# Kernel tuning notes

Hardware: AMD Instinct MI355X
Metric: run time of the kernel (lower is better)

Reference implementation:

```python
import jax, jax.numpy as jnp
import numpy as np

B, S, IN, E, H, FF, L = 8, 1024, 128, 512, 8, 2048, 4
HD = E // H
EPS = 1e-5


def make_pe(seq_len, d_model):
    position = np.arange(seq_len, dtype=np.float32)[:, None]
    div_term = np.exp(np.arange(0, d_model, 2, dtype=np.float32) * (-np.log(10000.0) / d_model))
    pe = np.zeros((seq_len, d_model), dtype=np.float32)
    pe[:, 0::2] = np.sin(position * div_term)
    pe[:, 1::2] = np.cos(position * div_term)
    return jnp.asarray(pe)


def setup_inputs() -> dict:
    key = jax.random.key(0)
    ks = jax.random.split(key, 16)
    s = 0.02
    return {
        "src": jax.random.normal(ks[0], (B, S, IN), jnp.float32),
        "distances": jax.random.uniform(ks[1], (B, S, S), jnp.float32),
        "proj_w": jax.random.normal(ks[2], (E, IN), jnp.float32) * s,
        "proj_b": jnp.zeros((E,), jnp.float32),
        "bn_g": jnp.ones((E,), jnp.float32),
        "bn_b": jnp.zeros((E,), jnp.float32),
        "in_proj_w": jax.random.normal(ks[3], (3 * E, E), jnp.float32) * s,
        "in_proj_b": jnp.zeros((3 * E,), jnp.float32),
        "dist_scale": jnp.array(1.0, jnp.float32),
        "lin1_w": jax.random.normal(ks[4], (FF, E), jnp.float32) * s,
        "lin1_b": jnp.zeros((FF,), jnp.float32),
        "lin2_w": jax.random.normal(ks[5], (E, FF), jnp.float32) * s,
        "lin2_b": jnp.zeros((E,), jnp.float32),
        "n1_g": jnp.ones((E,), jnp.float32),
        "n1_b": jnp.zeros((E,), jnp.float32),
        "n2_g": jnp.ones((E,), jnp.float32),
        "n2_b": jnp.zeros((E,), jnp.float32),
    }


def layernorm(x, g, b):
    m = jnp.mean(x, axis=-1, keepdims=True)
    v = jnp.var(x, axis=-1, keepdims=True)
    return (x - m) * jax.lax.rsqrt(v + EPS) * g + b


def reference(src, distances, proj_w, proj_b, bn_g, bn_b, in_proj_w, in_proj_b,
              dist_scale, lin1_w, lin1_b, lin2_w, lin2_b, n1_g, n1_b, n2_g, n2_b):
    # input projection
    x = jnp.einsum('bsi,ei->bse', src, proj_w) + proj_b  # [B,S,E]
    # BatchNorm1d over flattened (B*S) dim, training-mode batch stats
    xf = x.reshape(-1, E)
    mu = jnp.mean(xf, axis=0)
    var = jnp.var(xf, axis=0)
    x = ((xf - mu) * jax.lax.rsqrt(var + EPS) * bn_g + bn_b).reshape(B, S, E)
    # positional encoding
    x = x + make_pe(S, E)[None]
    # distance bias (same for every layer)
    dmax = jnp.max(distances, axis=-1, keepdims=True)
    dist_bias = jnp.exp(dist_scale * (1.0 - distances / dmax))  # [B,S,S]
    scale = 1.0 / jnp.sqrt(jnp.float32(HD))
    # num_layers iterations of the SAME (shared-parameter) layer
    for _ in range(L):
        qkv = jnp.einsum('bse,fe->bsf', x, in_proj_w) + in_proj_b  # [B,S,3E]
        q, k, v = jnp.split(qkv, 3, axis=-1)
        q = q.reshape(B, S, H, HD).transpose(0, 2, 1, 3)
        k = k.reshape(B, S, H, HD).transpose(0, 2, 1, 3)
        scores = jnp.einsum('bhqd,bhkd->bhqk', q, k) * scale  # [B,H,S,S]
        attn = jax.nn.softmax(scores, axis=-1)
        avg_w = jnp.mean(attn, axis=1)  # head-averaged weights [B,S,S]
        w = avg_w * dist_bias
        w = w / jnp.sum(w, axis=-1, keepdims=True)
        # NOTE: original bmm uses raw layer input as value (no V/out projection)
        attn_out = jnp.einsum('bqk,bke->bqe', w, x)
        x = layernorm(x + attn_out, n1_g, n1_b)
        ff = jnp.einsum('bsf,ef->bse', jax.nn.relu(jnp.einsum('bse,fe->bsf', x, lin1_w) + lin1_b), lin2_w) + lin2_b
        x = layernorm(x + ff, n2_g, n2_b)
    return x
```

## Files before the change

kernel.cpp:

```cpp
#include <hip/hip_runtime.h>
#include <hip/hip_bf16.h>
#include <math.h>

#define Bz 8
#define Sz 1024
#define INz 128
#define Ez 512
#define Hz 8
#define HDz 64
#define FFz 2048
#define Lz 4
#define Nz (Bz*Sz)
#define EPSf 1e-5f

typedef __attribute__((ext_vector_type(8))) short short8;
typedef __attribute__((ext_vector_type(4))) float floatx4;
#define MFMA16(a,b,c) __builtin_amdgcn_mfma_f32_16x16x32_bf16(a,b,c,0,0,0)

typedef __hip_bfloat16 bf16;

__device__ inline float b2f(bf16 v) { return __bfloat162float(v); }
__device__ inline bf16 f2b(float v) { return __float2bfloat16(v); }

__global__ __launch_bounds__(256) void cast_f2b(const float* __restrict__ in,
    bf16* __restrict__ out, int n)
{
  int i = blockIdx.x * 256 + threadIdx.x;
  if (i < n) out[i] = f2b(in[i]);
}

__global__ __launch_bounds__(256) void gemm_bt(
    const bf16* __restrict__ A, const bf16* __restrict__ Wm,
    const float* __restrict__ bias, float* __restrict__ Cf,
    bf16* __restrict__ Cb, const float* __restrict__ rowscale,
    int M, int N, int K, long sA, long sW, long sC, int relu)
{
  int z = blockIdx.z;
  A  += (size_t)z * sA;
  Wm += (size_t)z * sW;
  if (rowscale) rowscale += (size_t)z * M;
  size_t cbase = (size_t)z * sC;
  int bm = blockIdx.y * 128, bn = blockIdx.x * 128;
  __shared__ bf16 As[128][72];
  __shared__ bf16 Bs[128][72];
  int t = threadIdx.x, wave = t >> 6, lane = t & 63;
  int wm = (wave >> 1) * 64, wn = (wave & 1) * 64;
  int fr = lane & 15, fo = (lane >> 4) * 8;
  floatx4 acc[4][4];
  #pragma unroll
  for (int i = 0; i < 4; ++i)
    #pragma unroll
    for (int j = 0; j < 4; ++j) acc[i][j] = (floatx4){0.f, 0.f, 0.f, 0.f};

  for (int k0 = 0; k0 < K; k0 += 64) {
    #pragma unroll
    for (int i = 0; i < 4; ++i) {
      int idx = i * 256 + t, row = idx >> 3, c4 = idx & 7;
      *(float4*)&As[row][c4 * 8] = *(const float4*)(A  + (size_t)(bm + row) * K + k0 + c4 * 8);
      *(float4*)&Bs[row][c4 * 8] = *(const float4*)(Wm + (size_t)(bn + row) * K + k0 + c4 * 8);
    }
    __syncthreads();
    #pragma unroll
    for (int ks = 0; ks < 2; ++ks) {
      short8 af[4], bfv[4];
      #pragma unroll
      for (int rt = 0; rt < 4; ++rt) af[rt]  = *(const short8*)&As[wm + rt * 16 + fr][ks * 32 + fo];
      #pragma unroll
      for (int ct = 0; ct < 4; ++ct) bfv[ct] = *(const short8*)&Bs[wn + ct * 16 + fr][ks * 32 + fo];
      #pragma unroll
      for (int rt = 0; rt < 4; ++rt)
        #pragma unroll
        for (int ct = 0; ct < 4; ++ct)
          acc[rt][ct] = MFMA16(af[rt], bfv[ct], acc[rt][ct]);
    }
    __syncthreads();
  }
  #pragma unroll
  for (int rt = 0; rt < 4; ++rt) {
    #pragma unroll
    for (int r = 0; r < 4; ++r) {
      int row = bm + wm + rt * 16 + (lane >> 4) * 4 + r;
      float rs = rowscale ? (1.f / rowscale[row]) : 1.f;
      #pragma unroll
      for (int ct = 0; ct < 4; ++ct) {
        int col = bn + wn + ct * 16 + fr;
        float v = acc[rt][ct][r] + (bias ? bias[col] : 0.f);
        if (relu) v = fmaxf(v, 0.f);
        v *= rs;
        if (Cf) Cf[cbase + (size_t)row * N + col] = v;
        if (Cb) Cb[cbase + (size_t)row * N + col] = f2b(v);
      }
    }
  }
}

__global__ __launch_bounds__(256) void bn_stats(const float* __restrict__ x, float* __restrict__ st)
{
  int c = blockIdx.x;
  float s = 0.f, q = 0.f;
  for (int r = threadIdx.x; r < Nz; r += 256) {
    float v = x[(size_t)r * Ez + c];
    s += v; q += v * v;
  }
  for (int o = 32; o; o >>= 1) { s += __shfl_down(s, o); q += __shfl_down(q, o); }
  __shared__ float shs[4], shq[4];
  int w = threadIdx.x >> 6;
  if ((threadIdx.x & 63) == 0) { shs[w] = s; shq[w] = q; }
  __syncthreads();
  if (threadIdx.x == 0) {
    s = shs[0] + shs[1] + shs[2] + shs[3];
    q = shq[0] + shq[1] + shq[2] + shq[3];
    float mu = s / (float)Nz;
    float var = q / (float)Nz - mu * mu;
    st[c] = mu;
    st[Ez + c] = rsqrtf(var + EPSf);
  }
}

__global__ __launch_bounds__(256) void bn_apply_pe(const float* __restrict__ x0,
    const float* __restrict__ st, const float* __restrict__ g,
    const float* __restrict__ b, float* __restrict__ x, bf16* __restrict__ xb)
{
  int idx = blockIdx.x * 256 + threadIdx.x;
  int c = idx & (Ez - 1);
  int r = idx >> 9;
  int s = r & (Sz - 1);
  float dt = expf((float)(c & ~1) * (-9.210340371976184f / (float)Ez));
  float ang = (float)s * dt;
  float pe = (c & 1) ? cosf(ang) : sinf(ang);
  float mu = st[c], rs = st[Ez + c];
  float v = (x0[idx] - mu) * rs * g[c] + b[c] + pe;
  x[idx] = v;
  xb[idx] = f2b(v);
}

__global__ __launch_bounds__(256) void dist_bias_k(const float* __restrict__ dist,
    const float* __restrict__ dsc, bf16* __restrict__ db)
{
  size_t base = (size_t)blockIdx.x * Sz;
  float m = -1e30f;
  for (int j = threadIdx.x; j < Sz; j += 256) m = fmaxf(m, dist[base + j]);
  for (int o = 32; o; o >>= 1) m = fmaxf(m, __shfl_down(m, o));
  __shared__ float sh[4];
  if ((threadIdx.x & 63) == 0) sh[threadIdx.x >> 6] = m;
  __syncthreads();
  m = fmaxf(fmaxf(sh[0], sh[1]), fmaxf(sh[2], sh[3]));
  float sc = dsc[0];
  float inv = 1.f / m;
  for (int j = threadIdx.x; j < Sz; j += 256)
    db[base + j] = f2b(expf(sc * (1.f - dist[base + j] * inv)));
}

__global__ __launch_bounds__(256) void transpose_xb(const bf16* __restrict__ xb,
    bf16* __restrict__ xT)
{
  int b = blockIdx.z, e0 = blockIdx.y * 32, s0 = blockIdx.x * 32;
  __shared__ bf16 T[32][40];
  int t = threadIdx.x, row = t >> 3, c = t & 7;
  *(ushort4*)&T[row][c * 4] = *(const ushort4*)(xb + (size_t)(b * Sz + s0 + row) * Ez + e0 + c * 4);
  __syncthreads();
  ushort4 v;
  unsigned short* vp = (unsigned short*)&v;
  #pragma unroll
  for (int i = 0; i < 4; ++i) vp[i] = *(const unsigned short*)&T[c * 4 + i][row];
  *(ushort4*)(xT + ((size_t)b * Ez + e0 + row) * Sz + s0 + c * 4) = v;
}

__global__ __launch_bounds__(256) void attn_stats2(const bf16* __restrict__ qk,
    float* __restrict__ stats)
{
  int qt = blockIdx.x, h = blockIdx.y, b = blockIdx.z;
  int q0 = qt * 64;
  __shared__ bf16 Qs[64][72];
  __shared__ bf16 Ks[128][72];
  int t = threadIdx.x, wave = t >> 6, lane = t & 63;
  int fr = lane & 15, fo = (lane >> 4) * 8;
  #pragma unroll
  for (int i = 0; i < 2; ++i) {
    int idx = i * 256 + t, row = idx >> 3, c4 = idx & 7;
    *(float4*)&Qs[row][c4 * 8] =
      *(const float4*)(qk + (size_t)(b * Sz + q0 + row) * 1024 + h * 64 + c4 * 8);
  }
  __syncthreads();
  short8 aq0 = *(const short8*)&Qs[wave * 16 + fr][fo];
  short8 aq1 = *(const short8*)&Qs[wave * 16 + fr][32 + fo];
  float m_run[4] = {-1e30f, -1e30f, -1e30f, -1e30f};
  float z_run[4] = {0.f, 0.f, 0.f, 0.f};
  for (int k0 = 0; k0 < Sz; k0 += 128) {
    __syncthreads();
    #pragma unroll
    for (int i = 0; i < 4; ++i) {
      int idx = i * 256 + t, row = idx >> 3, c4 = idx & 7;
      *(float4*)&Ks[row][c4 * 8] =
        *(const float4*)(qk + (size_t)(b * Sz + k0 + row) * 1024 + 512 + h * 64 + c4 * 8);
    }
    __syncthreads();
    float sc[8][4];
    #pragma unroll
    for (int j = 0; j < 8; ++j) {
      floatx4 a4 = (floatx4){0.f, 0.f, 0.f, 0.f};
      short8 b0 = *(const short8*)&Ks[j * 16 + fr][fo];
      short8 b1 = *(const short8*)&Ks[j * 16 + fr][32 + fo];
      a4 = MFMA16(aq0, b0, a4);
      a4 = MFMA16(aq1, b1, a4);
      #pragma unroll
      for (int r = 0; r < 4; ++r) sc[j][r] = a4[r] * 0.125f;
    }
    #pragma unroll
    for (int r = 0; r < 4; ++r) {
      float vm = sc[0][r];
      #pragma unroll
      for (int j = 1; j < 8; ++j) vm = fmaxf(vm, sc[j][r]);
      #pragma unroll
      for (int o = 1; o < 16; o <<= 1) vm = fmaxf(vm, __shfl_xor(vm, o, 16));
      float mn = fmaxf(m_run[r], vm);
      float zb = 0.f;
      #pragma unroll
      for (int j = 0; j < 8; ++j) zb += __expf(sc[j][r] - mn);
      #pragma unroll
      for (int o = 1; o < 16; o <<= 1) zb += __shfl_xor(zb, o, 16);
      z_run[r] = z_run[r] * __expf(m_run[r] - mn) + zb;
      m_run[r] = mn;
    }
  }
  if (fr == 0) {
    int qb = q0 + wave * 16 + (lane >> 4) * 4;
    #pragma unroll
    for (int r = 0; r < 4; ++r) {
      size_t o = ((size_t)(b * Hz + h) * Sz + qb + r) * 2;
      stats[o] = m_run[r];
      stats[o + 1] = z_run[r];
    }
  }
}

__global__ __launch_bounds__(256) void scores_bias(const bf16* __restrict__ qk,
    const bf16* __restrict__ db, const float* __restrict__ stats,
    bf16* __restrict__ aw)
{
  int kt = blockIdx.x, qt = blockIdx.y, b = blockIdx.z;
  int q0 = qt * 32, k0 = kt * 32;
  __shared__ bf16 Qs[32][520];
  __shared__ bf16 Ks[32][520];
  __shared__ float mS[32][8], ziS[32][8];
  int t = threadIdx.x, wave = t >> 6, lane = t & 63;
  int fr = lane & 15, fo = (lane >> 4) * 8;
  #pragma unroll
  for (int i = 0; i < 8; ++i) {
    int idx = i * 256 + t, row = idx >> 6, c4 = idx & 63;
    *(float4*)&Qs[row][c4 * 8] = *(const float4*)(qk + (size_t)(b * Sz + q0 + row) * 1024 + c4 * 8);
    *(float4*)&Ks[row][c4 * 8] = *(const float4*)(qk + (size_t)(b * Sz + k0 + row) * 1024 + 512 + c4 * 8);
  }
  {
    int q = t >> 3, h = t & 7;
    size_t o = ((size_t)(b * Hz + h) * Sz + q0 + q) * 2;
    mS[q][h] = stats[o];
    ziS[q][h] = 1.f / stats[o + 1];
  }
  __syncthreads();
  int wq = (wave >> 1) * 16, wk = (wave & 1) * 16;
  floatx4 acch[8];
  #pragma unroll
  for (int h = 0; h < 8; ++h) {
    acch[h] = (floatx4){0.f, 0.f, 0.f, 0.f};
    #pragma unroll
    for (int ks = 0; ks < 2; ++ks) {
      short8 a = *(const short8*)&Qs[wq + fr][h * 64 + ks * 32 + fo];
      short8 bb = *(const short8*)&Ks[wk + fr][h * 64 + ks * 32 + fo];
      acch[h] = MFMA16(a, bb, acch[h]);
    }
  }
  #pragma unroll
  for (int r = 0; r < 4; ++r) {
    int qloc = wq + (lane >> 4) * 4 + r;
    int kloc = wk + fr;
    float p = 0.f;
    #pragma unroll
    for (int h = 0; h < 8; ++h)
      p += __expf(acch[h][r] * 0.125f - mS[qloc][h]) * ziS[qloc][h];
    size_t off = (size_t)(b * Sz + q0 + qloc) * Sz + k0 + kloc;
    p *= 0.125f * b2f(db[off]);
    aw[off] = f2b(p);
  }
}

__global__ __launch_bounds__(256) void rowsum(const bf16* __restrict__ aw,
    float* __restrict__ den)
{
  size_t base = (size_t)blockIdx.x * Sz;
  int t = threadIdx.x;
  ushort4 u = *(const ushort4*)(aw + base + t * 4);
  float s = __uint_as_float((unsigned)u.x << 16) + __uint_as_float((unsigned)u.y << 16)
          + __uint_as_float((unsigned)u.z << 16) + __uint_as_float((unsigned)u.w << 16);
  for (int o = 32; o; o >>= 1) s += __shfl_down(s, o);
  __shared__ float sh[4];
  if ((t & 63) == 0) sh[t >> 6] = s;
  __syncthreads();
  if (t == 0) den[blockIdx.x] = sh[0] + sh[1] + sh[2] + sh[3];
}

__global__ __launch_bounds__(256) void add_ln(const float* __restrict__ xin,
    const float* __restrict__ dly, const float* __restrict__ g,
    const float* __restrict__ bb, float* __restrict__ xout, bf16* __restrict__ xbout)
{
  size_t base = (size_t)blockIdx.x * Ez;
  int t = threadIdx.x;
  float a0 = xin[base + t] + dly[base + t];
  float a1 = xin[base + t + 256] + dly[base + t + 256];
  float s = a0 + a1, q = a0 * a0 + a1 * a1;
  for (int o = 32; o; o >>= 1) { s += __shfl_down(s, o); q += __shfl_down(q, o); }
  __shared__ float shs[4], shq[4];
  if ((t & 63) == 0) { shs[t >> 6] = s; shq[t >> 6] = q; }
  __syncthreads();
  s = shs[0] + shs[1] + shs[2] + shs[3];
  q = shq[0] + shq[1] + shq[2] + shq[3];
  float mu = s * (1.f / Ez);
  float var = q * (1.f / Ez) - mu * mu;
  float rs = rsqrtf(var + EPSf);
  float v0 = (a0 - mu) * rs * g[t] + bb[t];
  float v1 = (a1 - mu) * rs * g[t + 256] + bb[t + 256];
  xout[base + t] = v0;
  xout[base + t + 256] = v1;
  xbout[base + t] = f2b(v0);
  xbout[base + t + 256] = f2b(v1);
}

extern "C" void kernel_launch(void* const* d_in, const int* in_sizes, int n_in,
                              void* d_out, int out_size, void* d_ws, size_t ws_size,
                              hipStream_t stream)
{
  const float* src        = (const float*)d_in[0];
  const float* distances  = (const float*)d_in[1];
  const float* proj_w     = (const float*)d_in[2];
  const float* proj_b     = (const float*)d_in[3];
  const float* bn_g       = (const float*)d_in[4];
  const float* bn_b       = (const float*)d_in[5];
  const float* in_proj_w  = (const float*)d_in[6];
  const float* in_proj_b  = (const float*)d_in[7];
  const float* dist_scale = (const float*)d_in[8];
  const float* lin1_w     = (const float*)d_in[9];
  const float* lin1_b     = (const float*)d_in[10];
  const float* lin2_w     = (const float*)d_in[11];
  const float* lin2_b     = (const float*)d_in[12];
  const float* n1_g       = (const float*)d_in[13];
  const float* n1_b       = (const float*)d_in[14];
  const float* n2_g       = (const float*)d_in[15];
  const float* n2_b       = (const float*)d_in[16];

  float* x = (float*)d_out;

  float* stats = (float*)d_ws;
  float* den   = stats + 131072;
  float* bnst  = den + 8192;
  float* aout  = bnst + 1024;
  float* x0    = aout;
  bf16* db_b = (bf16*)(aout + (size_t)Nz * Ez);
  bf16* Rqk  = db_b + (size_t)Bz * Sz * Sz;
  bf16* qk   = Rqk;
  bf16* aw   = Rqk + (size_t)Nz * 1024;
  bf16* ff1  = Rqk;
  bf16* xb   = Rqk + (size_t)Nz * FFz;
  bf16* xT   = xb + (size_t)Nz * Ez;
  bf16* srcb = xT + (size_t)Bz * Ez * Sz;
  bf16* wpr  = srcb + (size_t)Nz * INz;
  bf16* wqk  = wpr + Ez * INz;
  bf16* wl1  = wqk + 1024 * Ez;
  bf16* wl2  = wl1 + FFz * Ez;

  cast_f2b<<<(Nz * INz) / 256, 256, 0, stream>>>(src, srcb, Nz * INz);
  cast_f2b<<<(Ez * INz + 255) / 256, 256, 0, stream>>>(proj_w, wpr, Ez * INz);
  cast_f2b<<<(1024 * Ez) / 256, 256, 0, stream>>>(in_proj_w, wqk, 1024 * Ez);
  cast_f2b<<<(FFz * Ez) / 256, 256, 0, stream>>>(lin1_w, wl1, FFz * Ez);
  cast_f2b<<<(Ez * FFz) / 256, 256, 0, stream>>>(lin2_w, wl2, Ez * FFz);

  gemm_bt<<<dim3(Ez / 128, Nz / 128, 1), 256, 0, stream>>>(
      srcb, wpr, proj_b, x0, nullptr, nullptr, Nz, Ez, INz, 0, 0, 0, 0);
  bn_stats<<<Ez, 256, 0, stream>>>(x0, bnst);
  bn_apply_pe<<<(Nz * Ez) / 256, 256, 0, stream>>>(x0, bnst, bn_g, bn_b, x, xb);
  dist_bias_k<<<Bz * Sz, 256, 0, stream>>>(distances, dist_scale, db_b);

  for (int l = 0; l < Lz; ++l) {
    transpose_xb<<<dim3(Sz / 32, Ez / 32, Bz), 256, 0, stream>>>(xb, xT);
    gemm_bt<<<dim3(1024 / 128, Nz / 128, 1), 256, 0, stream>>>(
        xb, wqk, in_proj_b, nullptr, qk, nullptr, Nz, 1024, Ez, 0, 0, 0, 0);
    attn_stats2<<<dim3(Sz / 64, Hz, Bz), 256, 0, stream>>>(qk, stats);
    scores_bias<<<dim3(Sz / 32, Sz / 32, Bz), 256, 0, stream>>>(qk, db_b, stats, aw);
    rowsum<<<Bz * Sz, 256, 0, stream>>>(aw, den);
    gemm_bt<<<dim3(Ez / 128, Sz / 128, Bz), 256, 0, stream>>>(
        aw, xT, nullptr, aout, nullptr, den,
        Sz, Ez, Sz, (long)Sz * Sz, (long)Ez * Sz, (long)Sz * Ez, 0);
    add_ln<<<Nz, 256, 0, stream>>>(x, aout, n1_g, n1_b, x, xb);
    gemm_bt<<<dim3(FFz / 128, Nz / 128, 1), 256, 0, stream>>>(
        xb, wl1, lin1_b, nullptr, ff1, nullptr, Nz, FFz, Ez, 0, 0, 0, 1);
    gemm_bt<<<dim3(Ez / 128, Nz / 128, 1), 256, 0, stream>>>(
        ff1, wl2, lin2_b, aout, nullptr, nullptr, Nz, Ez, FFz, 0, 0, 0, 0);
    add_ln<<<Nz, 256, 0, stream>>>(x, aout, n2_g, n2_b, x, xb);
  }
}
```

Measured before the change: 1.280 ms.

## Retile head-averaged score kernel to 128x128 tiles with per-head staging

New measurement: 1.238 ms. 1.03x faster.

```diff
diff --git a/kernel.cpp b/kernel.cpp
--- a/kernel.cpp
+++ b/kernel.cpp
@@ -239,48 +239,81 @@
     bf16* __restrict__ aw)
 {
   int kt = blockIdx.x, qt = blockIdx.y, b = blockIdx.z;
-  int q0 = qt * 32, k0 = kt * 32;
-  __shared__ bf16 Qs[32][520];
-  __shared__ bf16 Ks[32][520];
-  __shared__ float mS[32][8], ziS[32][8];
+  int q0 = qt * 128, k0 = kt * 128;
+  __shared__ bf16 Qs[128][72];
+  __shared__ bf16 Ks[128][72];
+  __shared__ float mS[128][9];
+  __shared__ float ziS[128][9];
   int t = threadIdx.x, wave = t >> 6, lane = t & 63;
   int fr = lane & 15, fo = (lane >> 4) * 8;
-  #pragma unroll
-  for (int i = 0; i < 8; ++i) {
-    int idx = i * 256 + t, row = idx >> 6, c4 = idx & 63;
-    *(float4*)&Qs[row][c4 * 8] = *(const float4*)(qk + (size_t)(b * Sz + q0 + row) * 1024 + c4 * 8);
-    *(float4*)&Ks[row][c4 * 8] = *(const float4*)(qk + (size_t)(b * Sz + k0 + row) * 1024 + 512 + c4 * 8);
-  }
-  {
-    int q = t >> 3, h = t & 7;
-    size_t o = ((size_t)(b * Hz + h) * Sz + q0 + q) * 2;
-    mS[q][h] = stats[o];
-    ziS[q][h] = 1.f / stats[o + 1];
-  }
-  __syncthreads();
-  int wq = (wave >> 1) * 16, wk = (wave & 1) * 16;
-  floatx4 acch[8];
-  #pragma unroll
+  int wm = (wave >> 1) * 64, wn = (wave & 1) * 64;
+
+  #pragma unroll
+  for (int i = 0; i < 4; ++i) {
+    int lin = i * 256 + t, h = lin >> 7, q = lin & 127;
+    const float* sp = stats + ((size_t)(b * Hz + h) * Sz + q0 + q) * 2;
+    mS[q][h] = sp[0];
+    ziS[q][h] = 1.f / sp[1];
+  }
+
+  floatx4 pac[4][4];
+  #pragma unroll
+  for (int i = 0; i < 4; ++i)
+    #pragma unroll
+    for (int j = 0; j < 4; ++j) pac[i][j] = (floatx4){0.f, 0.f, 0.f, 0.f};
+
   for (int h = 0; h < 8; ++h) {
-    acch[h] = (floatx4){0.f, 0.f, 0.f, 0.f};
-    #pragma unroll
-    for (int ks = 0; ks < 2; ++ks) {
-      short8 a = *(const short8*)&Qs[wq + fr][h * 64 + ks * 32 + fo];
-      short8 bb = *(const short8*)&Ks[wk + fr][h * 64 + ks * 32 + fo];
-      acch[h] = MFMA16(a, bb, acch[h]);
-    }
-  }
-  #pragma unroll
-  for (int r = 0; r < 4; ++r) {
-    int qloc = wq + (lane >> 4) * 4 + r;
-    int kloc = wk + fr;
-    float p = 0.f;
-    #pragma unroll
-    for (int h = 0; h < 8; ++h)
-      p += __expf(acch[h][r] * 0.125f - mS[qloc][h]) * ziS[qloc][h];
-    size_t off = (size_t)(b * Sz + q0 + qloc) * Sz + k0 + kloc;
-    p *= 0.125f * b2f(db[off]);
-    aw[off] = f2b(p);
+    __syncthreads();
+    #pragma unroll
+    for (int i = 0; i < 4; ++i) {
+      int idx = i * 256 + t, row = idx >> 3, c4 = idx & 7;
+      *(float4*)&Qs[row][c4 * 8] =
+        *(const float4*)(qk + (size_t)(b * Sz + q0 + row) * 1024 + h * 64 + c4 * 8);
+      *(float4*)&Ks[row][c4 * 8] =
+        *(const float4*)(qk + (size_t)(b * Sz + k0 + row) * 1024 + 512 + h * 64 + c4 * 8);
+    }
+    __syncthreads();
+    short8 bfv0[4], bfv1[4];
+    #pragma unroll
+    for (int ct = 0; ct < 4; ++ct) {
+      bfv0[ct] = *(const short8*)&Ks[wn + ct * 16 + fr][fo];
+      bfv1[ct] = *(const short8*)&Ks[wn + ct * 16 + fr][32 + fo];
+    }
+    #pragma unroll
+    for (int rt = 0; rt < 4; ++rt) {
+      short8 af0 = *(const short8*)&Qs[wm + rt * 16 + fr][fo];
+      short8 af1 = *(const short8*)&Qs[wm + rt * 16 + fr][32 + fo];
+      floatx4 sc[4];
+      #pragma unroll
+      for (int ct = 0; ct < 4; ++ct) {
+        floatx4 z4 = (floatx4){0.f, 0.f, 0.f, 0.f};
+        z4 = MFMA16(af0, bfv0[ct], z4);
+        sc[ct] = MFMA16(af1, bfv1[ct], z4);
+      }
+      #pragma unroll
+      for (int r = 0; r < 4; ++r) {
+        int qloc = wm + rt * 16 + (lane >> 4) * 4 + r;
+        float m = mS[qloc][h], zi = ziS[qloc][h];
+        #pragma unroll
+        for (int ct = 0; ct < 4; ++ct)
+          pac[rt][ct][r] += __expf(sc[ct][r] * 0.125f - m) * zi;
+      }
+    }
+  }
+
+  #pragma unroll
+  for (int rt = 0; rt < 4; ++rt) {
+    #pragma unroll
+    for (int r = 0; r < 4; ++r) {
+      int qloc = wm + rt * 16 + (lane >> 4) * 4 + r;
+      size_t rowoff = (size_t)(b * Sz + q0 + qloc) * Sz + k0;
+      #pragma unroll
+      for (int ct = 0; ct < 4; ++ct) {
+        int kloc = wn + ct * 16 + fr;
+        float p = pac[rt][ct][r] * 0.125f * b2f(db[rowoff + kloc]);
+        aw[rowoff + kloc] = f2b(p);
+      }
+    }
   }
 }
 
@@ -384,7 +417,7 @@
     gemm_bt<<<dim3(1024 / 128, Nz / 128, 1), 256, 0, stream>>>(
         xb, wqk, in_proj_b, nullptr, qk, nullptr, Nz, 1024, Ez, 0, 0, 0, 0);
     attn_stats2<<<dim3(Sz / 64, Hz, Bz), 256, 0, stream>>>(qk, stats);
-    scores_bias<<<dim3(Sz / 32, Sz / 32, Bz), 256, 0, stream>>>(qk, db_b, stats, aw);
+    scores_bias<<<dim3(Sz / 128, Sz / 128, Bz), 256, 0, stream>>>(qk, db_b, stats, aw);
     rowsum<<<Bz * Sz, 256, 0, stream>>>(aw, den);
     gemm_bt<<<dim3(Ez / 128, Sz / 128, Bz), 256, 0, stream>>>(
         aw, xT, nullptr, aout, nullptr, den,
```
